# Kernel optimization log

Hardware: AMD Instinct MI355X
Metric: run time of the kernel (lower is better)

Reference implementation:

```python
import jax, jax.numpy as jnp
import numpy as np

B, S, HID = 2, 8192, 1024
NH, DH, CL = 16, 64, 128
NB, NA = 1, 0  # num_chunks_before, num_chunks_after
NC = S // CL
MASK_VALUE = -1e9


def _look_adjacent(v):
    # v: [..., n_chunks, chunk_len(*d)] with chunk axis=2; torch's
    # cat([v[:,:,i:], v[:,:,:i]], dim=2) == jnp.roll(v, -i, axis=2)
    slices = [jnp.roll(v, -i, axis=2) for i in range(-NB, NA + 1)]
    return jnp.concatenate(slices, axis=3)


def setup_inputs() -> dict:
    key = jax.random.key(0)
    k1, k2, k3, k4 = jax.random.split(key, 4)
    scale = 1.0 / np.sqrt(HID).astype(np.float32)
    hidden_states = jax.random.normal(k1, (B, S, HID), jnp.float32)
    Wq = jax.random.normal(k2, (HID, NH * DH), jnp.float32) * scale
    Wk = jax.random.normal(k3, (HID, NH * DH), jnp.float32) * scale
    Wv = jax.random.normal(k4, (HID, NH * DH), jnp.float32) * scale
    return {"hidden_states": hidden_states, "Wq": Wq, "Wk": Wk, "Wv": Wv}


def _forward(hidden_states, Wq, Wk, Wv):
    # project and split heads -> [B, NH, NC, CL, DH]
    def proj(W):
        x = (hidden_states @ W).reshape(B, S, NH, DH)
        return x.transpose(0, 2, 1, 3).reshape(B, NH, NC, CL, DH)

    q = proj(Wq)
    k = proj(Wk) / jnp.sqrt(jnp.asarray(DH, hidden_states.dtype))
    v = proj(Wv)

    k_adj = _look_adjacent(k)  # [B, NH, NC, (NB+1+NA)*CL, DH]
    v_adj = _look_adjacent(v)

    # per-chunk scores: [B, NH, NC, CL, (NB+1+NA)*CL]
    dots = jnp.einsum("bhnqd,bhnkd->bhnqk", q, k_adj)

    # causal mask via position indices (decoder). Chunk 0's wrapped-around
    # keys carry large indices and are correctly masked out.
    idx = jnp.arange(S).reshape(1, 1, NC, CL)
    kv_idx = _look_adjacent(idx)  # [1, 1, NC, (NB+1+NA)*CL]
    causal = idx[..., :, None] >= kv_idx[..., None, :]
    dots = jnp.where(causal, dots, jnp.asarray(MASK_VALUE, dots.dtype))

    probs = jax.nn.softmax(dots, axis=-1)
    out = jnp.einsum("bhnqk,bhnkd->bhnqd", probs, v_adj)
    # merge chunks and heads -> [B, S, NH*DH]
    out = out.reshape(B, NH, S, DH).transpose(0, 2, 1, 3).reshape(B, S, NH * DH)
    return out


def reference(hidden_states, Wq, Wk, Wv):
    return _forward(hidden_states, Wq, Wk, Wv)
```

## Files before the change

kernel.cpp:

```cpp
#include <hip/hip_runtime.h>
#include <stdint.h>


typedef unsigned short u16;
typedef __bf16 bf16x8 __attribute__((ext_vector_type(8)));
typedef float f32x4 __attribute__((ext_vector_type(4)));

typedef __attribute__((address_space(1))) void* gas_ptr;
typedef __attribute__((address_space(3))) void* las_ptr;

__device__ __forceinline__ u16 f2bf(float f) {
  uint32_t u = __float_as_uint(f);
  u += 0x7fffu + ((u >> 16) & 1u);
  return (u16)(u >> 16);
}

__device__ __forceinline__ void gload16(const void* g, void* l) {
  __builtin_amdgcn_global_load_lds((gas_ptr)g, (las_ptr)l, 16, 0, 0);
}

__global__ void k_conv_x(const float* __restrict__ x, u16* __restrict__ o, int n4) {
  int i = blockIdx.x * blockDim.x + threadIdx.x;
  int stride = gridDim.x * blockDim.x;
  for (; i < n4; i += stride) {
    float4 v = reinterpret_cast<const float4*>(x)[i];
    unsigned long long pk = (unsigned long long)f2bf(v.x) |
                            ((unsigned long long)f2bf(v.y) << 16) |
                            ((unsigned long long)f2bf(v.z) << 32) |
                            ((unsigned long long)f2bf(v.w) << 48);
    reinterpret_cast<unsigned long long*>(o)[i] = pk;
  }
}

__global__ void k_conv_w(const float* __restrict__ wq, const float* __restrict__ wk,
                         const float* __restrict__ wv, u16* __restrict__ wt) {
  __shared__ float tile[32][33];
  int z = blockIdx.z;
  const float* src = (z == 0) ? wq : (z == 1) ? wk : wv;
  float scale = (z == 1) ? 0.125f : 1.0f;
  int n0 = blockIdx.x * 32, k0 = blockIdx.y * 32;
  int tx = threadIdx.x, ty = threadIdx.y;
  for (int i = ty; i < 32; i += 8)
    tile[i][tx] = src[(size_t)(k0 + i) * 1024 + n0 + tx];
  __syncthreads();
  u16* dst = wt + (size_t)z * 1024 * 1024;
  for (int i = ty; i < 32; i += 8)
    dst[(size_t)(n0 + i) * 1024 + k0 + tx] = f2bf(tile[tx][i] * scale);
}

__global__ __launch_bounds__(512, 2) void k_gemmf(const u16* __restrict__ xb,
                                                  const u16* __restrict__ wt,
                                                  u16* __restrict__ q_ws,
                                                  u16* __restrict__ k_ws,
                                                  u16* __restrict__ v_t) {
  __shared__ __align__(16) char lds[131072];
  char* As = lds;
  char* Bs = lds + 65536;
  const int tid = threadIdx.x;
  const int lane = tid & 63, l16 = lane & 15, lhi = lane >> 4;
  const int wave = tid >> 6;
  const int wm = (wave >> 2) * 128;
  const int wn = (wave & 3) * 64;

  const int bid = blockIdx.x;
  const int wg = (bid & 7) * 96 + (bid >> 3);
  const int mp = wg / 12;
  const int np = wg % 12;
  const int z = np >> 2;
  const int m0 = mp * 256;
  const int n0 = (np & 3) * 256;
  const u16* wz = wt + (size_t)z * 1024 * 1024;

  const int lrow8 = lane >> 3;
  const int scolx = ((lane & 7) * 16) ^ (lrow8 << 4);

  f32x4 acc[8][4] = {};

  auto stA = [&](int buf, int kt, int h) {
#pragma unroll
    for (int i = 0; i < 2; ++i) {
      int j = wave * 2 + i;
      int rb = 8 * j + 64 * (h + (j >> 3));
      int row = rb + lrow8;
      gload16((const char*)xb + ((size_t)(m0 + row) * 1024 + kt * 64) * 2 + scolx,
              As + buf * 32768 + rb * 128);
    }
  };
  auto stB = [&](int buf, int kt, int h) {
#pragma unroll
    for (int i = 0; i < 2; ++i) {
      int j = wave * 2 + i;
      int rb = 8 * (j & 3) + (j >> 2) * 64 + h * 32;
      int row = rb + lrow8;
      gload16((const char*)wz + ((size_t)(n0 + row) * 1024 + kt * 64) * 2 + scolx,
              Bs + buf * 32768 + rb * 128);
    }
  };

  stA(0, 0, 0); stB(0, 0, 0); stA(0, 0, 1); stB(0, 0, 1);

  const bool swapped = (z < 2);

  for (int t = 0; t < 16; ++t) {
    const int cbuf = t & 1, nbuf = cbuf ^ 1;
    const int ktn = (t < 15) ? t + 1 : 15;
    __syncthreads();
#pragma unroll
    for (int mh = 0; mh < 2; ++mh) {
      bf16x8 af[4][2];
#pragma unroll
      for (int fi = 0; fi < 4; ++fi) {
        int row = wm + (mh * 4 + fi) * 16 + l16;
#pragma unroll
        for (int ks = 0; ks < 2; ++ks)
          af[fi][ks] = *(const bf16x8*)(As + cbuf * 32768 + row * 128 +
                                        ((ks * 64 + lhi * 16) ^ ((row & 7) << 4)));
      }
#pragma unroll
      for (int nh = 0; nh < 2; ++nh) {
        bf16x8 bfr[2][2];
#pragma unroll
        for (int f2 = 0; f2 < 2; ++f2) {
          int rn = wn + nh * 32 + f2 * 16 + l16;
#pragma unroll
          for (int ks = 0; ks < 2; ++ks)
            bfr[f2][ks] = *(const bf16x8*)(Bs + cbuf * 32768 + rn * 128 +
                                           ((ks * 64 + lhi * 16) ^ ((rn & 7) << 4)));
        }
        int p = mh * 2 + nh;
        if (p == 0) stA(nbuf, ktn, 0);
        else if (p == 1) stB(nbuf, ktn, 0);
        else if (p == 2) stA(nbuf, ktn, 1);
        else stB(nbuf, ktn, 1);
        __builtin_amdgcn_s_setprio(1);
        if (swapped) {
#pragma unroll
          for (int fi = 0; fi < 4; ++fi)
#pragma unroll
            for (int f2 = 0; f2 < 2; ++f2)
#pragma unroll
              for (int ks = 0; ks < 2; ++ks)
                acc[mh * 4 + fi][nh * 2 + f2] = __builtin_amdgcn_mfma_f32_16x16x32_bf16(
                    bfr[f2][ks], af[fi][ks], acc[mh * 4 + fi][nh * 2 + f2], 0, 0, 0);
        } else {
#pragma unroll
          for (int fi = 0; fi < 4; ++fi)
#pragma unroll
            for (int f2 = 0; f2 < 2; ++f2)
#pragma unroll
              for (int ks = 0; ks < 2; ++ks)
                acc[mh * 4 + fi][nh * 2 + f2] = __builtin_amdgcn_mfma_f32_16x16x32_bf16(
                    af[fi][ks], bfr[f2][ks], acc[mh * 4 + fi][nh * 2 + f2], 0, 0, 0);
        }
        __builtin_amdgcn_s_setprio(0);
      }
    }
  }

  if (swapped) {
    u16* o = (z == 0) ? q_ws : k_ws;
#pragma unroll
    for (int fr = 0; fr < 8; ++fr) {
#pragma unroll
      for (int fn = 0; fn < 4; ++fn) {
        int m = m0 + wm + fr * 16 + l16;
        int n = n0 + wn + fn * 16 + lhi * 4;
        unsigned long long pk = (unsigned long long)f2bf(acc[fr][fn][0]) |
                                ((unsigned long long)f2bf(acc[fr][fn][1]) << 16) |
                                ((unsigned long long)f2bf(acc[fr][fn][2]) << 32) |
                                ((unsigned long long)f2bf(acc[fr][fn][3]) << 48);
        *(unsigned long long*)((char*)o + ((size_t)m * 1024 + n) * 2) = pk;
      }
    }
  } else {
#pragma unroll
    for (int fr = 0; fr < 8; ++fr) {
#pragma unroll
      for (int fn = 0; fn < 4; ++fn) {
        int m = m0 + wm + fr * 16 + lhi * 4;
        int n = n0 + wn + fn * 16 + l16;
        int bb = m >> 13;
        int s = m & 8191;
        unsigned long long pk = (unsigned long long)f2bf(acc[fr][fn][0]) |
                                ((unsigned long long)f2bf(acc[fr][fn][1]) << 16) |
                                ((unsigned long long)f2bf(acc[fr][fn][2]) << 32) |
                                ((unsigned long long)f2bf(acc[fr][fn][3]) << 48);
        *(unsigned long long*)((char*)v_t + ((size_t)(bb * 1024 + n) * 8192 + s) * 2) = pk;
      }
    }
  }
}

__global__ __launch_bounds__(256, 3) void k_attn(const u16* __restrict__ qw,
                                                 const u16* __restrict__ kw,
                                                 const u16* __restrict__ vt,
                                                 float* __restrict__ out) {
  __shared__ __align__(16) char lds[32768];
  char* k_s = lds;
  const int tid = threadIdx.x;
  const int lane = tid & 63, l16 = lane & 15, lhi = lane >> 4;
  const int wave = tid >> 6;
  char* p_s = lds + wave * 8192;
  const int c = blockIdx.x & 63;
  const int h = (blockIdx.x >> 6) & 15;
  const int b = blockIdx.x >> 10;
  const int cprev = (c == 0) ? 0 : c - 1;
  const int dstb = (tid & 192) * 16;

#pragma unroll
  for (int it = 0; it < 8; ++it) {
    int idx = it * 256 + tid;
    int row = idx >> 3, colb = (idx & 7) * 16;
    int srow = (row < 128) ? (cprev * 128 + row) : (c * 128 + row - 128);
    gload16((const char*)kw + ((size_t)(b * 8192 + srow) * 1024 + h * 64) * 2 +
                (colb ^ ((row & 7) << 4)),
            k_s + it * 4096 + dstb);
  }

  const int rbase = wave * 32;
  bf16x8 qf[2][2];
#pragma unroll
  for (int rb = 0; rb < 2; ++rb)
#pragma unroll
    for (int ks = 0; ks < 2; ++ks)
      qf[rb][ks] = *(const bf16x8*)((const char*)qw +
                                    ((size_t)(b * 8192 + c * 128 + rbase + rb * 16 + l16)) * 2048 +
                                    h * 128 + ks * 64 + lhi * 16);

  __syncthreads();

  f32x4 accs[2][16];
#pragma unroll
  for (int rb = 0; rb < 2; ++rb)
#pragma unroll
    for (int nb = 0; nb < 16; ++nb) accs[rb][nb] = f32x4{0.f, 0.f, 0.f, 0.f};

#pragma unroll
  for (int ks = 0; ks < 2; ++ks) {
#pragma unroll
    for (int nb = 0; nb < 16; ++nb) {
      int row = nb * 16 + l16;
      bf16x8 bfb = *(const bf16x8*)(k_s + row * 128 + ((ks * 64 + lhi * 16) ^ ((row & 7) << 4)));
#pragma unroll
      for (int rb = 0; rb < 2; ++rb)
        accs[rb][nb] = __builtin_amdgcn_mfma_f32_16x16x32_bf16(qf[rb][ks], bfb, accs[rb][nb], 0, 0, 0);
    }
  }

  float rinv[2][4];
#pragma unroll
  for (int rb = 0; rb < 2; ++rb) {
#pragma unroll
    for (int j = 0; j < 4; ++j) {
      int qi = rbase + rb * 16 + lhi * 4 + j;
      float m = -3.0e38f;
#pragma unroll
      for (int nb = 0; nb < 16; ++nb) {
        int kl = nb * 16 + l16;
        float v = accs[rb][nb][j];
        bool valid = (kl <= qi + 128) && ((c > 0) || (kl >= 128));
        v = valid ? v : -1.0e9f;
        accs[rb][nb][j] = v;
        m = fmaxf(m, v);
      }
#pragma unroll
      for (int d = 1; d < 16; d <<= 1) m = fmaxf(m, __shfl_xor(m, d));
      float s = 0.f;
#pragma unroll
      for (int nb = 0; nb < 16; ++nb) {
        float e = __expf(accs[rb][nb][j] - m);
        accs[rb][nb][j] = e;
        s += e;
      }
#pragma unroll
      for (int d = 1; d < 16; d <<= 1) s += __shfl_xor(s, d);
      rinv[rb][j] = 1.0f / s;
    }
  }

  __syncthreads();

  f32x4 acco[2][4] = {};
#pragma unroll
  for (int half = 0; half < 2; ++half) {
#pragma unroll
    for (int rb = 0; rb < 2; ++rb) {
#pragma unroll
      for (int nbh = 0; nbh < 8; ++nbh) {
#pragma unroll
        for (int j = 0; j < 4; ++j) {
          int r = rb * 16 + lhi * 4 + j;
          int cb = (nbh * 16 + l16) * 2;
          *(u16*)(p_s + r * 256 + (cb ^ ((r & 7) << 4))) = f2bf(accs[rb][half * 8 + nbh][j]);
        }
      }
    }
    __asm__ volatile("s_waitcnt lgkmcnt(0)" ::: "memory");
    __builtin_amdgcn_sched_barrier(0);
#pragma unroll
    for (int ks = 0; ks < 4; ++ks) {
      bf16x8 pf[2];
#pragma unroll
      for (int rb = 0; rb < 2; ++rb) {
        int r = rb * 16 + l16;
        pf[rb] = *(const bf16x8*)(p_s + r * 256 + ((ks * 64 + lhi * 16) ^ ((r & 7) << 4)));
      }
#pragma unroll
      for (int db = 0; db < 4; ++db) {
        int vr = db * 16 + l16;
        size_t koffb = c ? ((size_t)(c - 1) * 256 + half * 256 + ks * 64 + lhi * 16)
                         : (size_t)((half * 256 + ks * 64 + lhi * 16) & 255);
        bf16x8 vf = *(const bf16x8*)((const char*)vt +
                                     ((size_t)((b * 16 + h) * 64 + vr)) * 16384 + koffb);
#pragma unroll
        for (int rb = 0; rb < 2; ++rb)
          acco[rb][db] = __builtin_amdgcn_mfma_f32_16x16x32_bf16(pf[rb], vf, acco[rb][db], 0, 0, 0);
      }
    }
    if (half == 0) {
      __asm__ volatile("s_waitcnt lgkmcnt(0)" ::: "memory");
      __builtin_amdgcn_sched_barrier(0);
    }
  }

#pragma unroll
  for (int rb = 0; rb < 2; ++rb) {
#pragma unroll
    for (int db = 0; db < 4; ++db) {
#pragma unroll
      for (int j = 0; j < 4; ++j) {
        int r = rbase + rb * 16 + lhi * 4 + j;
        out[(size_t)(b * 8192 + c * 128 + r) * 1024 + h * 64 + db * 16 + l16] =
            acco[rb][db][j] * rinv[rb][j];
      }
    }
  }
}

extern "C" void kernel_launch(void* const* d_in, const int* in_sizes, int n_in,
                              void* d_out, int out_size, void* d_ws, size_t ws_size,
                              hipStream_t stream) {
  const float* hs = (const float*)d_in[0];
  const float* wq = (const float*)d_in[1];
  const float* wk = (const float*)d_in[2];
  const float* wv = (const float*)d_in[3];
  float* out = (float*)d_out;
  char* ws = (char*)d_ws;

  u16* x_bf = (u16*)ws;
  u16* wt   = (u16*)(ws + 33554432);
  u16* q_ws = (u16*)(ws + 39845888);
  u16* k_ws = (u16*)(ws + 73400320);
  u16* v_t  = (u16*)(ws + 106954752);

  k_conv_x<<<dim3(2048), dim3(256), 0, stream>>>(hs, x_bf, 16384 * 1024 / 4);
  k_conv_w<<<dim3(32, 32, 3), dim3(32, 8), 0, stream>>>(wq, wk, wv, wt);
  k_gemmf<<<dim3(768), dim3(512), 0, stream>>>(x_bf, wt, q_ws, k_ws, v_t);
  k_attn<<<dim3(2048), dim3(256), 0, stream>>>(q_ws, k_ws, v_t, out);
}
```

Baseline: 344.6 us.

## Stage Q and V tiles in LDS for attention, batch GEMM prefetch issue

In the attention kernel, Q and the transposed V window are now loaded asynchronously into swizzled LDS alongside K, replacing direct per-lane global reads during the score and PV MFMA loops. LDS use grows to 80KB, so the occupancy hint drops from 3 to 2 blocks per CU. In the projection GEMM, the next tile's A/B loads are now issued all at once right after the barrier, using precomputed base offsets, instead of being interleaved with the MFMA sub-steps. The goal is to avoid exposed global latency in the inner loops, at the cost of fewer resident blocks and less fine-grained overlap in the GEMM.

```diff
diff --git a/kernel.cpp b/kernel.cpp
--- a/kernel.cpp
+++ b/kernel.cpp
@@ -74,30 +74,31 @@
   const int lrow8 = lane >> 3;
   const int scolx = ((lane & 7) * 16) ^ (lrow8 << 4);
 
+  const int j0 = wave * 2, j1 = wave * 2 + 1;
+  const int rbA00 = 8 * j0 + 64 * (0 + (j0 >> 3)), rbA01 = 8 * j1 + 64 * (0 + (j1 >> 3));
+  const int rbA10 = 8 * j0 + 64 * (1 + (j0 >> 3)), rbA11 = 8 * j1 + 64 * (1 + (j1 >> 3));
+  const int rbB00 = 8 * (j0 & 3) + (j0 >> 2) * 64, rbB01 = 8 * (j1 & 3) + (j1 >> 2) * 64;
+  const int rbB10 = rbB00 + 32, rbB11 = rbB01 + 32;
+  const char* aB = (const char*)xb + (size_t)m0 * 2048 + scolx;
+  const char* bB = (const char*)wz + (size_t)n0 * 2048 + scolx;
+
   f32x4 acc[8][4] = {};
 
-  auto stA = [&](int buf, int kt, int h) {
-#pragma unroll
-    for (int i = 0; i < 2; ++i) {
-      int j = wave * 2 + i;
-      int rb = 8 * j + 64 * (h + (j >> 3));
-      int row = rb + lrow8;
-      gload16((const char*)xb + ((size_t)(m0 + row) * 1024 + kt * 64) * 2 + scolx,
-              As + buf * 32768 + rb * 128);
-    }
+  auto stageAll = [&](int buf, int kt) {
+    const size_t ko = (size_t)kt * 128;
+    char* Ad = As + buf * 32768;
+    char* Bd = Bs + buf * 32768;
+    gload16(aB + (size_t)(rbA00 + lrow8) * 2048 + ko, Ad + rbA00 * 128);
+    gload16(aB + (size_t)(rbA01 + lrow8) * 2048 + ko, Ad + rbA01 * 128);
+    gload16(aB + (size_t)(rbA10 + lrow8) * 2048 + ko, Ad + rbA10 * 128);
+    gload16(aB + (size_t)(rbA11 + lrow8) * 2048 + ko, Ad + rbA11 * 128);
+    gload16(bB + (size_t)(rbB00 + lrow8) * 2048 + ko, Bd + rbB00 * 128);
+    gload16(bB + (size_t)(rbB01 + lrow8) * 2048 + ko, Bd + rbB01 * 128);
+    gload16(bB + (size_t)(rbB10 + lrow8) * 2048 + ko, Bd + rbB10 * 128);
+    gload16(bB + (size_t)(rbB11 + lrow8) * 2048 + ko, Bd + rbB11 * 128);
   };
-  auto stB = [&](int buf, int kt, int h) {
-#pragma unroll
-    for (int i = 0; i < 2; ++i) {
-      int j = wave * 2 + i;
-      int rb = 8 * (j & 3) + (j >> 2) * 64 + h * 32;
-      int row = rb + lrow8;
-      gload16((const char*)wz + ((size_t)(n0 + row) * 1024 + kt * 64) * 2 + scolx,
-              Bs + buf * 32768 + rb * 128);
-    }
-  };
-
-  stA(0, 0, 0); stB(0, 0, 0); stA(0, 0, 1); stB(0, 0, 1);
+
+  stageAll(0, 0);
 
   const bool swapped = (z < 2);
 
@@ -105,6 +106,7 @@
     const int cbuf = t & 1, nbuf = cbuf ^ 1;
     const int ktn = (t < 15) ? t + 1 : 15;
     __syncthreads();
+    stageAll(nbuf, ktn);
 #pragma unroll
     for (int mh = 0; mh < 2; ++mh) {
       bf16x8 af[4][2];
@@ -127,11 +129,6 @@
             bfr[f2][ks] = *(const bf16x8*)(Bs + cbuf * 32768 + rn * 128 +
                                            ((ks * 64 + lhi * 16) ^ ((rn & 7) << 4)));
         }
-        int p = mh * 2 + nh;
-        if (p == 0) stA(nbuf, ktn, 0);
-        else if (p == 1) stB(nbuf, ktn, 0);
-        else if (p == 2) stA(nbuf, ktn, 1);
-        else stB(nbuf, ktn, 1);
         __builtin_amdgcn_s_setprio(1);
         if (swapped) {
 #pragma unroll
@@ -191,12 +188,14 @@
   }
 }
 
-__global__ __launch_bounds__(256, 3) void k_attn(const u16* __restrict__ qw,
+__global__ __launch_bounds__(256, 2) void k_attn(const u16* __restrict__ qw,
                                                  const u16* __restrict__ kw,
                                                  const u16* __restrict__ vt,
                                                  float* __restrict__ out) {
-  __shared__ __align__(16) char lds[32768];
-  char* k_s = lds;
+  __shared__ __align__(16) char lds[81920];
+  char* q_s = lds;
+  char* k_s = lds + 16384;
+  char* v_s = lds + 49152;
   const int tid = threadIdx.x;
   const int lane = tid & 63, l16 = lane & 15, lhi = lane >> 4;
   const int wave = tid >> 6;
@@ -208,6 +207,14 @@
   const int dstb = (tid & 192) * 16;
 
 #pragma unroll
+  for (int it = 0; it < 4; ++it) {
+    int idx = it * 256 + tid;
+    int row = idx >> 3, colb = (idx & 7) * 16;
+    gload16((const char*)qw + ((size_t)(b * 8192 + c * 128 + row) * 1024 + h * 64) * 2 +
+                (colb ^ ((row & 7) << 4)),
+            q_s + it * 4096 + dstb);
+  }
+#pragma unroll
   for (int it = 0; it < 8; ++it) {
     int idx = it * 256 + tid;
     int row = idx >> 3, colb = (idx & 7) * 16;
@@ -216,34 +223,40 @@
                 (colb ^ ((row & 7) << 4)),
             k_s + it * 4096 + dstb);
   }
+#pragma unroll
+  for (int it = 0; it < 8; ++it) {
+    int idx = it * 256 + tid;
+    int row = idx >> 5;
+    int colb = (idx & 31) * 16;
+    int colbl = colb ^ ((row & 7) << 4);
+    size_t roff = ((size_t)((b * 16 + h) * 64 + row)) * 8192 * 2;
+    size_t soff = c ? ((size_t)(c * 128 - 128) * 2 + colbl) : (size_t)(colbl & 255);
+    gload16((const char*)vt + roff + soff, v_s + it * 4096 + dstb);
+  }
+  __syncthreads();
 
   const int rbase = wave * 32;
-  bf16x8 qf[2][2];
+  f32x4 accs[2][16];
 #pragma unroll
   for (int rb = 0; rb < 2; ++rb)
 #pragma unroll
-    for (int ks = 0; ks < 2; ++ks)
-      qf[rb][ks] = *(const bf16x8*)((const char*)qw +
-                                    ((size_t)(b * 8192 + c * 128 + rbase + rb * 16 + l16)) * 2048 +
-                                    h * 128 + ks * 64 + lhi * 16);
-
-  __syncthreads();
-
-  f32x4 accs[2][16];
-#pragma unroll
-  for (int rb = 0; rb < 2; ++rb)
-#pragma unroll
     for (int nb = 0; nb < 16; ++nb) accs[rb][nb] = f32x4{0.f, 0.f, 0.f, 0.f};
 
 #pragma unroll
   for (int ks = 0; ks < 2; ++ks) {
+    bf16x8 af[2];
+#pragma unroll
+    for (int rb = 0; rb < 2; ++rb) {
+      int row = rbase + rb * 16 + l16;
+      af[rb] = *(const bf16x8*)(q_s + row * 128 + ((ks * 64 + lhi * 16) ^ ((row & 7) << 4)));
+    }
 #pragma unroll
     for (int nb = 0; nb < 16; ++nb) {
       int row = nb * 16 + l16;
       bf16x8 bfb = *(const bf16x8*)(k_s + row * 128 + ((ks * 64 + lhi * 16) ^ ((row & 7) << 4)));
 #pragma unroll
       for (int rb = 0; rb < 2; ++rb)
-        accs[rb][nb] = __builtin_amdgcn_mfma_f32_16x16x32_bf16(qf[rb][ks], bfb, accs[rb][nb], 0, 0, 0);
+        accs[rb][nb] = __builtin_amdgcn_mfma_f32_16x16x32_bf16(af[rb], bfb, accs[rb][nb], 0, 0, 0);
     }
   }
 
@@ -308,10 +321,8 @@
 #pragma unroll
       for (int db = 0; db < 4; ++db) {
         int vr = db * 16 + l16;
-        size_t koffb = c ? ((size_t)(c - 1) * 256 + half * 256 + ks * 64 + lhi * 16)
-                         : (size_t)((half * 256 + ks * 64 + lhi * 16) & 255);
-        bf16x8 vf = *(const bf16x8*)((const char*)vt +
-                                     ((size_t)((b * 16 + h) * 64 + vr)) * 16384 + koffb);
+        bf16x8 vf = *(const bf16x8*)(v_s + vr * 512 +
+                                     ((half * 256 + ks * 64 + lhi * 16) ^ ((vr & 7) << 4)));
 #pragma unroll
         for (int rb = 0; rb < 2; ++rb)
           acco[rb][db] = __builtin_amdgcn_mfma_f32_16x16x32_bf16(pf[rb], vf, acco[rb][db], 0, 0, 0);
```

Result: faster. 301.9 us (-12.4%).
